# Kernel optimization log

Measured on AMD Instinct MI355X. Metric: run time of the kernel, lower is better.

The kernel has to match this reference:

```python
import jax, jax.numpy as jnp
import numpy as np

H, D = 8, 32            # num_heads, per-head out_dim (same for C1/C2/C3/state)
ALPHA = 0.2             # leaky-relu negative slope
N_C, N_S = 10000, 1024  # nodes per C type, state nodes
E_CC, E_CS = 120000, 10000
IN_C, IN_S = 128, 64


def setup_inputs() -> dict:
    key = jax.random.key(0)
    ks = jax.random.split(key, 20)
    xn = lambda k, sh, s=1.0: jax.random.normal(k, sh, dtype=jnp.float32) * s
    inp = {}
    inp["feat_C1"] = xn(ks[0], (N_C, IN_C))
    inp["feat_C2"] = xn(ks[1], (N_C, IN_C))
    inp["feat_C3"] = xn(ks[2], (N_C, IN_C))
    inp["feat_state"] = xn(ks[3], (N_S, IN_S))
    # linear weights (xavier-ish scale) and zero biases
    inp["W_node"] = xn(ks[4], (3, IN_C, H * D), 0.06)
    inp["b_node"] = jnp.zeros((3, H * D), jnp.float32)
    inp["W_cc"] = xn(ks[5], (9, IN_C, H * D), 0.06)
    inp["b_cc"] = jnp.zeros((9, H * D), jnp.float32)
    inp["W_cs"] = xn(ks[6], (3, IN_C, H * D), 0.06)
    inp["b_cs"] = jnp.zeros((3, H * D), jnp.float32)
    inp["W_in"] = xn(ks[7], (IN_S, H * D), 0.08)
    inp["b_in"] = jnp.zeros((H * D,), jnp.float32)
    # attention vectors: [..., 0] = src vec, [..., 1] = dst vec
    inp["attn_cc"] = xn(ks[8], (9, 2, H, D), 0.3)
    inp["attn_cs"] = xn(ks[9], (3, 2, H, D), 0.3)
    # edge lists; relation r = 3*src_type + dst_type for cc
    inp["edges_cc_src"] = jax.random.randint(ks[10], (9, E_CC), 0, N_C, dtype=jnp.int32)
    inp["edges_cc_dst"] = jax.random.randint(ks[11], (9, E_CC), 0, N_C, dtype=jnp.int32)
    inp["edges_cs_src"] = jax.random.randint(ks[12], (3, E_CS), 0, N_C, dtype=jnp.int32)
    inp["edges_cs_dst"] = jax.random.randint(ks[13], (3, E_CS), 0, N_S, dtype=jnp.int32)
    return inp


def _segment_softmax(e, dst, n):
    # e: [E, H]; softmax over edges sharing the same dst node (DGL edge_softmax)
    m = jax.ops.segment_max(e, dst, num_segments=n)
    ex = jnp.exp(e - m[dst])
    s = jax.ops.segment_sum(ex, dst, num_segments=n)
    return ex / s[dst]


def _gat_relation(Wh_src, Wh_dst_self, a_src_vec, a_dst_vec, src, dst, n_dst):
    # Wh_src: [Ns,H,D] projected src feats for this relation
    # Wh_dst_self: [Nd,H,D] dst-type self projection (used for dst attention)
    a_s = jnp.sum(Wh_src * a_src_vec, axis=-1)       # [Ns,H]
    a_d = jnp.sum(Wh_dst_self * a_dst_vec, axis=-1)  # [Nd,H]
    e = jax.nn.leaky_relu(a_s[src] + a_d[dst], ALPHA)   # [E,H]
    a = _segment_softmax(e, dst, n_dst)                 # [E,H]
    msg = Wh_src[src] * a[:, :, None]                   # [E,H,D]
    return jax.ops.segment_sum(msg, dst, num_segments=n_dst)


def _forward(feat_C1, feat_C2, feat_C3, feat_state, W_node, b_node, W_cc, b_cc,
             W_cs, b_cs, W_in, b_in, attn_cc, attn_cs,
             edges_cc_src, edges_cc_dst, edges_cs_src, edges_cs_dst):
    feats_c = [feat_C1, feat_C2, feat_C3]
    n_c = [f.shape[0] for f in feats_c]
    # self projections (used as dst attention features)
    Wh_node = [(feats_c[t] @ W_node[t] + b_node[t]).reshape(-1, H, D) for t in range(3)]
    out_c = [jnp.zeros_like(Wh_node[t]) for t in range(3)]
    # 9 C->C relations: r = 3*s + d
    for r in range(9):
        s, d = divmod(r, 3)
        Wh = (feats_c[s] @ W_cc[r] + b_cc[r]).reshape(-1, H, D)
        ft = _gat_relation(Wh, Wh_node[d], attn_cc[r, 0], attn_cc[r, 1],
                           edges_cc_src[r], edges_cc_dst[r], n_c[d])
        out_c[d] = out_c[d] + ft
    # state: 'in' self projection + 3 C->state relations
    Wh_in = (feat_state @ W_in + b_in).reshape(-1, H, D)
    out_s = Wh_in
    n_s = feat_state.shape[0]
    for t in range(3):
        Wh = (feats_c[t] @ W_cs[t] + b_cs[t]).reshape(-1, H, D)
        ft = _gat_relation(Wh, Wh_in, attn_cs[t, 0], attn_cs[t, 1],
                           edges_cs_src[t], edges_cs_dst[t], n_s)
        out_s = out_s + ft
    relu = jax.nn.relu
    return (relu(out_c[0]), relu(out_c[1]), relu(out_c[2]), relu(out_s))


def reference(feat_C1, feat_C2, feat_C3, feat_state, W_node, b_node, W_cc, b_cc,
              W_cs, b_cs, W_in, b_in, attn_cc, attn_cs,
              edges_cc_src, edges_cc_dst, edges_cs_src, edges_cs_dst):
    return _forward(feat_C1, feat_C2, feat_C3, feat_state, W_node, b_node, W_cc,
                    b_cc, W_cs, b_cs, W_in, b_in, attn_cc, attn_cs,
                    edges_cc_src, edges_cc_dst, edges_cs_src, edges_cs_dst)
```

## Files before the change

kernel.cpp:

```cpp
#include <hip/hip_runtime.h>


#define H_ 8
#define D_ 32
#define HD 256
#define NC 10000
#define NS 1024
#define INC 128
#define INS 64
#define ECC 120000
#define ECS 10000
#define ALPHA 0.2f
#define CAP 64

typedef unsigned short u16;
typedef __attribute__((ext_vector_type(8))) short short8;
typedef __attribute__((ext_vector_type(4))) float f32x4;
typedef __attribute__((ext_vector_type(2))) float f32x2;

static constexpr size_t WHB_CC = 0;
static constexpr size_t WHB_CS = 23040000;
static constexpr size_t WHB_IN = 30720000;
static constexpr size_t FB0  = 15491072;
static constexpr size_t ASCC = FB0;
static constexpr size_t ADCC = FB0 + 720000;
static constexpr size_t ASCS = FB0 + 1440000;
static constexpr size_t ADCS = FB0 + 1680000;
static constexpr size_t BAF  = FB0 + 1704576;
static constexpr size_t FBC  = 34437760;
static constexpr size_t FBS  = 38277760;
static constexpr size_t WTCC = 38343296;
static constexpr size_t WTCS = 38638208;
static constexpr size_t WTIN = 38736512;
static constexpr size_t WAT  = 38752896;
static constexpr size_t IBYTE = 77768704;
static constexpr size_t SBYTE = 78140992;

static constexpr int TOTE  = 9 * ECC + 3 * ECS;
static constexpr int NB_Z0 = 91;
static constexpr int NB_FT = 3814;
static constexpr int NB_WT = 104;
static constexpr int NB_FO = 32;
static constexpr int NB_K2 = 2710;

__device__ __forceinline__ u16 f2b(float f) {
  unsigned u = __float_as_uint(f);
  return (u16)((u + 0x7FFFu + ((u >> 16) & 1u)) >> 16);
}
__device__ __forceinline__ float bl(unsigned u) { return __uint_as_float(u << 16); }
__device__ __forceinline__ float bh(unsigned u) { return __uint_as_float(u & 0xffff0000u); }

__global__ __launch_bounds__(256) void k_prep(
    const float* f1, const float* f2, const float* f3, const float* fs,
    const float* Wcc, const float* Wcs, const float* Win, const float* Wnode,
    const float* bcc, const float* bnode, const float* bcs, const float* bin,
    const float* accv, const float* acsv,
    u16* wsu, float* wsf, int* cnts) {
  __shared__ float Ls[64 * 65];
  int b = blockIdx.x, t = threadIdx.x;
  if (b < NB_Z0) {
    int i = b * 256 + t;
    if (i < 23268) ((int4*)cnts)[i] = make_int4(0, 0, 0, 0);
    return;
  }
  b -= NB_Z0;
  if (b < NB_FT) {
    const float* src; u16* dst; int idx, n4;
    if (b < 3750) {
      int ty = b / 1250;
      src = (ty == 0) ? f1 : (ty == 1) ? f2 : f3;
      dst = wsu + FBC + (size_t)ty * 1280000;
      idx = (b - ty * 1250) * 256 + t; n4 = 320000;
    } else {
      src = fs; dst = wsu + FBS; idx = (b - 3750) * 256 + t; n4 = 16384;
    }
    if (idx < n4) {
      float4 v = ((const float4*)src)[idx];
      uint2 o;
      o.x = (unsigned)f2b(v.x) | ((unsigned)f2b(v.y) << 16);
      o.y = (unsigned)f2b(v.z) | ((unsigned)f2b(v.w) << 16);
      *(uint2*)(dst + (size_t)idx * 4) = o;
    }
    return;
  }
  b -= NB_FT;
  if (b < NB_WT) {
    int mat = b >> 3, sub = b & 7;
    int K = (mat == 12) ? INS : INC;
    if (mat == 12 && sub >= 4) return;
    int k0 = (sub >> 2) * 64, n0 = (sub & 3) * 64;
    const float* src; u16* dst;
    if (mat < 9)        { src = Wcc + (size_t)mat * INC * HD;        dst = wsu + WTCC + (size_t)mat * 32768; }
    else if (mat < 12)  { src = Wcs + (size_t)(mat - 9) * INC * HD;  dst = wsu + WTCS + (size_t)(mat - 9) * 32768; }
    else                { src = Win;                                 dst = wsu + WTIN; }
    #pragma unroll
    for (int it = 0; it < 4; it++) {
      int idx = t + it * 256;
      int r = idx >> 4, c4 = idx & 15;
      float4 v = *(const float4*)&src[(size_t)(k0 + r) * HD + n0 + c4 * 4];
      Ls[r * 65 + c4 * 4 + 0] = v.x; Ls[r * 65 + c4 * 4 + 1] = v.y;
      Ls[r * 65 + c4 * 4 + 2] = v.z; Ls[r * 65 + c4 * 4 + 3] = v.w;
    }
    __syncthreads();
    int n = t >> 2, k8 = (t & 3) * 16;
    unsigned o[8];
    #pragma unroll
    for (int j = 0; j < 8; j++) {
      u16 lo = f2b(Ls[(k8 + 2 * j) * 65 + n]);
      u16 hi = f2b(Ls[(k8 + 2 * j + 1) * 65 + n]);
      o[j] = (unsigned)lo | ((unsigned)hi << 16);
    }
    uint4* dp = (uint4*)&dst[(size_t)(n0 + n) * K + k0 + k8];
    dp[0] = make_uint4(o[0], o[1], o[2], o[3]);
    dp[1] = make_uint4(o[4], o[5], o[6], o[7]);
    return;
  }
  b -= NB_WT;
  int tile = b >> 3, sub = b & 7;
  int K = (tile == 3) ? INS : INC;
  int c0 = sub * 8;
  for (int idx = t; idx < 8 * K; idx += 256) {
    int col = c0 + idx / K, k = idx % K;
    int m = col >> 3, h = col & 7;
    const float* W = nullptr; const float* av = nullptr;
    if (tile < 3) {
      if (m < 3)      { int r = 3*tile + m; W = Wcc + (size_t)r*INC*HD;   av = accv + (size_t)r*512 + h*32; }
      else if (m < 6) { int r = 3*(m-3) + tile; W = Wnode + (size_t)tile*INC*HD; av = accv + (size_t)r*512 + 256 + h*32; }
      else if (m == 6){ W = Wcs + (size_t)tile*INC*HD; av = acsv + (size_t)tile*512 + h*32; }
    } else if (m < 3) { W = Win; av = acsv + (size_t)m*512 + 256 + h*32; }
    float s = 0.f;
    if (W) {
      const float* wp = W + (size_t)k * HD + h * 32;
      #pragma unroll 8
      for (int d = 0; d < 32; d++) s += wp[d] * av[d];
    }
    wsu[WAT + (size_t)tile * 8192 + (size_t)col * K + k] = f2b(s);
  }
  if (sub == 0 && t < 64) {
    int col = t, m = col >> 3, h = col & 7;
    const float* bb = nullptr; const float* av = nullptr;
    if (tile < 3) {
      if (m < 3)      { int r = 3*tile + m; bb = bcc + (size_t)r*HD;  av = accv + (size_t)r*512 + h*32; }
      else if (m < 6) { int r = 3*(m-3) + tile; bb = bnode + (size_t)tile*HD; av = accv + (size_t)r*512 + 256 + h*32; }
      else if (m == 6){ bb = bcs + (size_t)tile*HD; av = acsv + (size_t)tile*512 + h*32; }
    } else if (m < 3) { bb = bin; av = acsv + (size_t)m*512 + 256 + h*32; }
    float s = 0.f;
    if (bb) for (int d = 0; d < 32; d++) s += bb[h*32 + d] * av[d];
    wsf[BAF + tile * 64 + col] = s;
  }
}

__global__ __launch_bounds__(256, 2) void k_fuse(
    u16* wsu, float* wsf, const float* bcc, const float* bcs, const float* bin,
    const int* eccs, const int* eccd, const int* ecss, const int* ecsd,
    int* cnts, u16* slt) {
  __shared__ __align__(16) char smem[69632];
  int gb = blockIdx.x, t = threadIdx.x;
  if ((gb % 5) == 4) {
    int k = gb / 5;
    int i0 = (k * 256 + t) * 8;
    if (i0 >= TOTE) return;
    int dd[8], ss[8], p[8];
    int cbase;
    if (i0 < 9 * ECC) {
      int r = i0 / ECC;
      int4 d0 = *(const int4*)&eccd[i0]; int4 d1 = *(const int4*)&eccd[i0 + 4];
      int4 s0 = *(const int4*)&eccs[i0]; int4 s1 = *(const int4*)&eccs[i0 + 4];
      dd[0]=d0.x; dd[1]=d0.y; dd[2]=d0.z; dd[3]=d0.w;
      dd[4]=d1.x; dd[5]=d1.y; dd[6]=d1.z; dd[7]=d1.w;
      ss[0]=s0.x; ss[1]=s0.y; ss[2]=s0.z; ss[3]=s0.w;
      ss[4]=s1.x; ss[5]=s1.y; ss[6]=s1.z; ss[7]=s1.w;
      cbase = r * NC;
    } else {
      int u0 = i0 - 9 * ECC;
      int r = u0 / ECS;
      int4 d0 = *(const int4*)&ecsd[u0]; int4 d1 = *(const int4*)&ecsd[u0 + 4];
      int4 s0 = *(const int4*)&ecss[u0]; int4 s1 = *(const int4*)&ecss[u0 + 4];
      dd[0]=d0.x; dd[1]=d0.y; dd[2]=d0.z; dd[3]=d0.w;
      dd[4]=d1.x; dd[5]=d1.y; dd[6]=d1.z; dd[7]=d1.w;
      ss[0]=s0.x; ss[1]=s0.y; ss[2]=s0.z; ss[3]=s0.w;
      ss[4]=s1.x; ss[5]=s1.y; ss[6]=s1.z; ss[7]=s1.w;
      cbase = 90000 + r * NS;
    }
    #pragma unroll
    for (int q = 0; q < 8; q++) p[q] = atomicAdd(&cnts[cbase + dd[q]], 1);
    #pragma unroll
    for (int q = 0; q < 8; q++)
      if (p[q] < CAP) slt[((size_t)(cbase + dd[q])) * CAP + p[q]] = (u16)ss[q];
    return;
  }
  int g = 4 * (gb / 5) + (gb % 5);
  if (g >= 2157) return;
  u16* As = (u16*)smem;
  u16* Bs = (u16*)(smem + 34816);
  const u16 *A, *Bt; const float* bias = nullptr; u16* C = nullptr;
  int M, K, r0, n0 = 0, ty = 0;
  bool isScore = false;
  if (g < 1896) {
    int z = g / 158, rem = g - z * 158;
    int by = rem / 79, bx = rem - by * 79;
    r0 = bx * 128; n0 = by * 128; M = NC; K = 128;
    if (z < 9) { A = wsu + FBC + (size_t)(z/3)*1280000; Bt = wsu + WTCC + (size_t)z*32768; bias = bcc + (size_t)z*HD; C = wsu + WHB_CC + (size_t)z*NC*HD; }
    else { int q = z - 9; A = wsu + FBC + (size_t)q*1280000; Bt = wsu + WTCS + (size_t)q*32768; bias = bcs + (size_t)q*HD; C = wsu + WHB_CS + (size_t)q*NC*HD; }
  } else if (g < 1912) {
    int loc = g - 1896; int by = loc / 8, bx = loc - by * 8;
    r0 = bx * 128; n0 = by * 128; M = NS; K = 64;
    A = wsu + FBS; Bt = wsu + WTIN; bias = bin; C = wsu + WHB_IN;
  } else if (g < 2149) {
    isScore = true; ty = (g - 1912) / 79; int bx = (g - 1912) % 79;
    r0 = bx * 128; M = NC; K = 128;
    A = wsu + FBC + (size_t)ty * 1280000; Bt = wsu + WAT + (size_t)ty * 8192;
  } else {
    isScore = true; ty = 3; int bx = g - 2149;
    r0 = bx * 128; M = NS; K = 64;
    A = wsu + FBS; Bt = wsu + WAT + (size_t)3 * 8192;
  }
  int SA = K + 8;
  int NB = isScore ? 64 : 128;
  {
    int ksh = (K == 128) ? 4 : 3;
    int kmask = (1 << ksh) - 1;
    int sc8 = SA >> 3;
    const uint4* ga = (const uint4*)(A + (size_t)r0 * K);
    const uint4* gb2 = (const uint4*)(Bt + (size_t)n0 * K);
    uint4* la = (uint4*)As; uint4* lb = (uint4*)Bs;
    int tota = (128 * K) >> 3, totb = (NB * K) >> 3;
    for (int i = t; i < tota; i += 256) la[(i >> ksh) * sc8 + (i & kmask)] = ga[i];
    for (int i = t; i < totb; i += 256) lb[(i >> ksh) * sc8 + (i & kmask)] = gb2[i];
  }
  __syncthreads();
  int lane = t & 63, w = t >> 6, l16 = lane & 15, quad = lane >> 4;
  int arow0 = w * 32 + l16;
  if (!isScore) {
    f32x4 acc[2][8];
    #pragma unroll
    for (int i = 0; i < 2; i++)
      #pragma unroll
      for (int j = 0; j < 8; j++) acc[i][j] = (f32x4){0.f, 0.f, 0.f, 0.f};
    for (int ks = 0; ks < K; ks += 32) {
      int ko = ks + quad * 8;
      short8 a0 = *(const short8*)&As[(size_t)arow0 * SA + ko];
      short8 a1 = *(const short8*)&As[(size_t)(arow0 + 16) * SA + ko];
      #pragma unroll
      for (int j = 0; j < 8; j++) {
        short8 bfr = *(const short8*)&Bs[(size_t)(j * 16 + l16) * SA + ko];
        acc[0][j] = __builtin_amdgcn_mfma_f32_16x16x32_bf16(a0, bfr, acc[0][j], 0, 0, 0);
        acc[1][j] = __builtin_amdgcn_mfma_f32_16x16x32_bf16(a1, bfr, acc[1][j], 0, 0, 0);
      }
    }
    __syncthreads();
    float* Cl = (float*)smem;
    #pragma unroll
    for (int i = 0; i < 2; i++) {
      int rl0 = w * 32 + i * 16 + quad * 4;
      #pragma unroll
      for (int j = 0; j < 8; j++) {
        int cl = j * 16 + l16;
        float bv = bias[n0 + cl];
        #pragma unroll
        for (int rg = 0; rg < 4; rg++)
          Cl[(rl0 + rg) * 132 + cl] = acc[i][j][rg] + bv;
      }
    }
    __syncthreads();
    for (int task = t; task < 2048; task += 256) {
      int row = task >> 4, seg = task & 15;
      int gr = r0 + row;
      if (gr >= M) continue;
      const float* cp = Cl + row * 132 + seg * 8;
      float4 v0 = *(const float4*)cp;
      float4 v1 = *(const float4*)(cp + 4);
      uint4 o;
      o.x = (unsigned)f2b(v0.x) | ((unsigned)f2b(v0.y) << 16);
      o.y = (unsigned)f2b(v0.z) | ((unsigned)f2b(v0.w) << 16);
      o.z = (unsigned)f2b(v1.x) | ((unsigned)f2b(v1.y) << 16);
      o.w = (unsigned)f2b(v1.z) | ((unsigned)f2b(v1.w) << 16);
      *(uint4*)&C[(size_t)gr * HD + n0 + seg * 8] = o;
    }
  } else {
    f32x4 acc[2][4];
    #pragma unroll
    for (int i = 0; i < 2; i++)
      #pragma unroll
      for (int j = 0; j < 4; j++) acc[i][j] = (f32x4){0.f, 0.f, 0.f, 0.f};
    for (int ks = 0; ks < K; ks += 32) {
      int ko = ks + quad * 8;
      short8 a0 = *(const short8*)&As[(size_t)arow0 * SA + ko];
      short8 a1 = *(const short8*)&As[(size_t)(arow0 + 16) * SA + ko];
      #pragma unroll
      for (int j = 0; j < 4; j++) {
        short8 bfr = *(const short8*)&Bs[(size_t)(j * 16 + l16) * SA + ko];
        acc[0][j] = __builtin_amdgcn_mfma_f32_16x16x32_bf16(a0, bfr, acc[0][j], 0, 0, 0);
        acc[1][j] = __builtin_amdgcn_mfma_f32_16x16x32_bf16(a1, bfr, acc[1][j], 0, 0, 0);
      }
    }
    float* sp[4]; float bav[4];
    #pragma unroll
    for (int j = 0; j < 4; j++) {
      int col = j * 16 + l16;
      int m = col >> 3, h = col & 7;
      float* p = nullptr;
      if (ty < 3) {
        if (m < 3)       p = wsf + ASCC + (size_t)(3*ty + m) * NC * H_;
        else if (m < 6)  p = wsf + ADCC + (size_t)(3*(m-3) + ty) * NC * H_;
        else if (m == 6) p = wsf + ASCS + (size_t)ty * NC * H_;
      } else if (m < 3)  p = wsf + ADCS + (size_t)m * NS * H_;
      sp[j] = p ? (p + h) : nullptr;
      bav[j] = wsf[BAF + ty * 64 + col];
    }
    #pragma unroll
    for (int i = 0; i < 2; i++) {
      int rl0 = w * 32 + i * 16 + quad * 4;
      #pragma unroll
      for (int j = 0; j < 4; j++) {
        if (!sp[j]) continue;
        #pragma unroll
        for (int rg = 0; rg < 4; rg++) {
          int gr = r0 + rl0 + rg;
          if (gr < M) sp[j][(size_t)gr * 8] = (acc[i][j][rg] + bav[j]) * 1.44269504089f;
        }
      }
    }
  }
}

__global__ __launch_bounds__(256) void k_agg(const u16* wsu, const float* wsf,
                                             const int* cnts, const u16* slt,
                                             float* out) {
  int t = threadIdx.x, lane = t & 63, w = t >> 6;
  int borig = blockIdx.x;
  int xcd = borig & 7, pos = borig >> 3;
  int sb = (xcd < 4) ? xcd * 970 + pos : 3880 + (xcd - 4) * 969 + pos;
  int node = sb * 4 + w;
  int l3 = lane >> 3, h7 = lane & 7;
  int lb = lane * 8;
  f32x2 totA = {0.f, 0.f}, totB = {0.f, 0.f};
  bool isC = node < 3 * NC;
  int dtype = 0, n;
  if (isC) { dtype = node / NC; n = node - dtype * NC; } else { n = node - 3 * NC; }
  for (int j = 0; j < 3; j++) {
    int cidx; const float* ASp; const float* ADp; const char* wb;
    if (isC) {
      int r = j * 3 + dtype;
      cidx = r * NC + n;
      ASp = wsf + ASCC + (size_t)r * NC * H_;
      ADp = wsf + ADCC + (size_t)r * NC * H_;
      wb  = (const char*)(wsu + WHB_CC + (size_t)r * NC * HD);
    } else {
      cidx = 90000 + j * NS + n;
      ASp = wsf + ASCS + (size_t)j * NC * H_;
      ADp = wsf + ADCS + (size_t)j * NS * H_;
      wb  = (const char*)(wsu + WHB_CS + (size_t)j * NC * HD);
    }
    int cnt = min(cnts[cidx], CAP);
    if (cnt <= 0) continue;
    int srcid = (int)slt[(size_t)cidx * CAP + min(lane, cnt - 1)];
    float adn = ADp[(size_t)n * H_ + h7];
    f32x2 aA = {0.f, 0.f}, aB = {0.f, 0.f};
    float zac = 0.f;
    float wcur;
    {
      int ce = min(l3, cnt - 1);
      int sid = __shfl(srcid, ce);
      float sc = ASp[(size_t)sid * H_ + h7] + adn;
      sc = fmaxf(sc, ALPHA * sc);
      wcur = (l3 < cnt) ? __builtin_amdgcn_exp2f(sc) : 0.f;
    }
    for (int g = 0; g < cnt; g += 8) {
      uint2 mreg[8];
      #pragma unroll
      for (int ee = 0; ee < 8; ee++) {
        int ce = min(g + ee, cnt - 1);
        int sre = __builtin_amdgcn_readlane(srcid, ce);
        mreg[ee] = *(const uint2*)(wb + ((size_t)(unsigned)sre << 9) + lb);
      }
      float wold = wcur;
      zac += wold;
      if (g + 8 < cnt) {
        int e = g + 8 + l3;
        int ce = min(e, cnt - 1);
        int sid = __shfl(srcid, ce);
        float sc = ASp[(size_t)sid * H_ + h7] + adn;
        sc = fmaxf(sc, ALPHA * sc);
        wcur = (e < cnt) ? __builtin_amdgcn_exp2f(sc) : 0.f;
      }
      #pragma unroll
      for (int ee = 0; ee < 8; ee++) {
        float we = __shfl(wold, ee * 8 + l3);
        f32x2 q0, q1;
        q0.x = bl(mreg[ee].x); q0.y = bh(mreg[ee].x);
        q1.x = bl(mreg[ee].y); q1.y = bh(mreg[ee].y);
        aA += q0 * we;
        aB += q1 * we;
      }
    }
    zac += __shfl_xor(zac, 8);
    zac += __shfl_xor(zac, 16);
    zac += __shfl_xor(zac, 32);
    float inv = 1.f / zac;
    float invp = __shfl(inv, l3);
    totA += aA * invp;
    totB += aB * invp;
  }
  if (!isC) {
    uint2 m = *(const uint2*)((const char*)(wsu + WHB_IN) + (size_t)n * 512 + lb);
    totA.x += bl(m.x); totA.y += bh(m.x);
    totB.x += bl(m.y); totB.y += bh(m.y);
  }
  float4 v = make_float4(fmaxf(totA.x, 0.f), fmaxf(totA.y, 0.f),
                         fmaxf(totB.x, 0.f), fmaxf(totB.y, 0.f));
  *(float4*)(out + (size_t)node * HD + lane * 4) = v;
}

extern "C" void kernel_launch(void* const* d_in, const int* in_sizes, int n_in,
                              void* d_out, int out_size, void* d_ws, size_t ws_size,
                              hipStream_t stream) {
  (void)in_sizes; (void)n_in; (void)out_size; (void)ws_size;
  const float* f1    = (const float*)d_in[0];
  const float* f2    = (const float*)d_in[1];
  const float* f3    = (const float*)d_in[2];
  const float* fs    = (const float*)d_in[3];
  const float* Wnode = (const float*)d_in[4];
  const float* bnode = (const float*)d_in[5];
  const float* Wcc   = (const float*)d_in[6];
  const float* bcc   = (const float*)d_in[7];
  const float* Wcs   = (const float*)d_in[8];
  const float* bcs   = (const float*)d_in[9];
  const float* Win   = (const float*)d_in[10];
  const float* bin   = (const float*)d_in[11];
  const float* accv  = (const float*)d_in[12];
  const float* acsv  = (const float*)d_in[13];
  const int* eccs    = (const int*)d_in[14];
  const int* eccd    = (const int*)d_in[15];
  const int* ecss    = (const int*)d_in[16];
  const int* ecsd    = (const int*)d_in[17];
  float* wsf = (float*)d_ws;
  u16*   wsu = (u16*)d_ws;
  int*   cnts = (int*)((char*)d_ws + IBYTE);
  u16*   slt  = (u16*)((char*)d_ws + SBYTE);
  float* out = (float*)d_out;

  k_prep<<<dim3(NB_Z0 + NB_FT + NB_WT + NB_FO), 256, 0, stream>>>(
      f1, f2, f3, fs, Wcc, Wcs, Win, Wnode, bcc, bnode, bcs, bin, accv, acsv,
      wsu, wsf, cnts);
  k_fuse<<<dim3(NB_K2), 256, 0, stream>>>(
      wsu, wsf, bcc, bcs, bin, eccs, eccd, ecss, ecsd, cnts, slt);
  k_agg<<<dim3((3 * NC + NS) / 4), 256, 0, stream>>>(wsu, wsf, cnts, slt, out);
}
```

Measured before the change: 250.7 us.

## Bucket incoming edge slots by source-node window to improve gather locality

Edge bucketing now splits each destination's 64 slots into four 16-slot windows keyed by source id range, using a packed byte-per-window atomic counter. The aggregation kernel walks windows in order, gathering four rows at a time. The goal is more ordered and cache-friendly gathers of projected source features. In exchange, gathers are issued in smaller batches, and a window that receives more than 16 edges silently drops the extras, which is a correctness risk.

Result: slower. 256.7 us (+2.4%).

```diff
diff --git a/kernel.cpp b/kernel.cpp
--- a/kernel.cpp
+++ b/kernel.cpp
@@ -12,6 +12,8 @@
 #define ECS 10000
 #define ALPHA 0.2f
 #define CAP 64
+#define CAPW 16
+#define NWIN 4
 
 typedef unsigned short u16;
 typedef __attribute__((ext_vector_type(8))) short short8;
@@ -49,6 +51,9 @@
 }
 __device__ __forceinline__ float bl(unsigned u) { return __uint_as_float(u << 16); }
 __device__ __forceinline__ float bh(unsigned u) { return __uint_as_float(u & 0xffff0000u); }
+__device__ __forceinline__ int srcwin(int s) {
+  return (s >= 2500) + (s >= 5000) + (s >= 7500);
+}
 
 __global__ __launch_bounds__(256) void k_prep(
     const float* f1, const float* f2, const float* f3, const float* fs,
@@ -182,11 +187,18 @@
       ss[4]=s1.x; ss[5]=s1.y; ss[6]=s1.z; ss[7]=s1.w;
       cbase = 90000 + r * NS;
     }
-    #pragma unroll
-    for (int q = 0; q < 8; q++) p[q] = atomicAdd(&cnts[cbase + dd[q]], 1);
+    int wn[8];
+    #pragma unroll
+    for (int q = 0; q < 8; q++) wn[q] = srcwin(ss[q]);
     #pragma unroll
     for (int q = 0; q < 8; q++)
-      if (p[q] < CAP) slt[((size_t)(cbase + dd[q])) * CAP + p[q]] = (u16)ss[q];
+      p[q] = atomicAdd(&cnts[cbase + dd[q]], 1 << (wn[q] * 8));
+    #pragma unroll
+    for (int q = 0; q < 8; q++) {
+      int pq = (p[q] >> (wn[q] * 8)) & 255;
+      if (pq < CAPW)
+        slt[((size_t)(cbase + dd[q])) * CAP + wn[q] * CAPW + pq] = (u16)ss[q];
+    }
     return;
   }
   int g = 4 * (gb / 5) + (gb % 5);
@@ -322,6 +334,16 @@
       }
     }
   }
+}
+
+__device__ __forceinline__ float score8w(const float* ASp, float adn, int srcv,
+                                         int win, int base, int cw,
+                                         int l3, int h7) {
+  int e = base + l3;
+  int sid = __shfl(srcv, win * CAPW + min(e, cw - 1));
+  float sc = ASp[(size_t)sid * H_ + h7] + adn;
+  sc = fmaxf(sc, ALPHA * sc);
+  return (e < cw) ? __builtin_amdgcn_exp2f(sc) : 0.f;
 }
 
 __global__ __launch_bounds__(256) void k_agg(const u16* wsu, const float* wsf,
@@ -352,46 +374,38 @@
       ADp = wsf + ADCS + (size_t)j * NS * H_;
       wb  = (const char*)(wsu + WHB_CS + (size_t)j * NC * HD);
     }
-    int cnt = min(cnts[cidx], CAP);
-    if (cnt <= 0) continue;
-    int srcid = (int)slt[(size_t)cidx * CAP + min(lane, cnt - 1)];
+    int pcnt = cnts[cidx];
+    if (pcnt == 0) continue;
+    int srcv = (int)slt[(size_t)cidx * CAP + lane];
     float adn = ADp[(size_t)n * H_ + h7];
     f32x2 aA = {0.f, 0.f}, aB = {0.f, 0.f};
     float zac = 0.f;
-    float wcur;
-    {
-      int ce = min(l3, cnt - 1);
-      int sid = __shfl(srcid, ce);
-      float sc = ASp[(size_t)sid * H_ + h7] + adn;
-      sc = fmaxf(sc, ALPHA * sc);
-      wcur = (l3 < cnt) ? __builtin_amdgcn_exp2f(sc) : 0.f;
-    }
-    for (int g = 0; g < cnt; g += 8) {
-      uint2 mreg[8];
-      #pragma unroll
-      for (int ee = 0; ee < 8; ee++) {
-        int ce = min(g + ee, cnt - 1);
-        int sre = __builtin_amdgcn_readlane(srcid, ce);
-        mreg[ee] = *(const uint2*)(wb + ((size_t)(unsigned)sre << 9) + lb);
-      }
-      float wold = wcur;
-      zac += wold;
-      if (g + 8 < cnt) {
-        int e = g + 8 + l3;
-        int ce = min(e, cnt - 1);
-        int sid = __shfl(srcid, ce);
-        float sc = ASp[(size_t)sid * H_ + h7] + adn;
-        sc = fmaxf(sc, ALPHA * sc);
-        wcur = (e < cnt) ? __builtin_amdgcn_exp2f(sc) : 0.f;
-      }
-      #pragma unroll
-      for (int ee = 0; ee < 8; ee++) {
-        float we = __shfl(wold, ee * 8 + l3);
-        f32x2 q0, q1;
-        q0.x = bl(mreg[ee].x); q0.y = bh(mreg[ee].x);
-        q1.x = bl(mreg[ee].y); q1.y = bh(mreg[ee].y);
-        aA += q0 * we;
-        aB += q1 * we;
+    for (int win = 0; win < NWIN; win++) {
+      int cw = min((pcnt >> (win * 8)) & 255, CAPW);
+      if (cw == 0) continue;
+      float wcur = score8w(ASp, adn, srcv, win, 0, cw, l3, h7);
+      zac += wcur;
+      for (int g = 0; g < cw; g += 4) {
+        if (g == 8) {
+          wcur = score8w(ASp, adn, srcv, win, 8, cw, l3, h7);
+          zac += wcur;
+        }
+        uint2 mreg[4];
+        #pragma unroll
+        for (int ee = 0; ee < 4; ee++) {
+          int sre = __builtin_amdgcn_readlane(
+              srcv, win * CAPW + min(g + ee, cw - 1));
+          mreg[ee] = *(const uint2*)(wb + ((size_t)(unsigned)sre << 9) + lb);
+        }
+        #pragma unroll
+        for (int ee = 0; ee < 4; ee++) {
+          float we = __shfl(wcur, ((g + ee) & 7) * 8 + l3);
+          f32x2 q0, q1;
+          q0.x = bl(mreg[ee].x); q0.y = bh(mreg[ee].x);
+          q1.x = bl(mreg[ee].y); q1.y = bh(mreg[ee].y);
+          aA += q0 * we;
+          aB += q1 * we;
+        }
       }
     }
     zac += __shfl_xor(zac, 8);
```
